# Performance work log

Measured on AMD Instinct MI355X. Metric: run time of the kernel, lower is better.

Reference implementation:

```python
import jax, jax.numpy as jnp
import numpy as np

K = 50  # hard-coded top-k in the original module


def setup_inputs() -> dict:
    key = jax.random.key(0)
    k1, k2 = jax.random.split(key)
    N = 16777216  # 2**24
    logit = jax.random.uniform(k1, (N,), dtype=jnp.float32)
    mv = jax.random.uniform(k2, (N,), dtype=jnp.float32)
    return {"logit": logit, "mv": mv}


def reference(logit, mv):
    dt = logit.dtype
    l1 = jnp.abs(logit - mv)
    _, idx = jax.lax.top_k(mv, K)

    # rank weights: base (detached mv + 0.5)*0.5; top-k entries scaled by
    # 2 * (((k - i)/k)**3 * 4 + 1) where i is the rank position.
    rank_w = (jax.lax.stop_gradient(mv) + 0.5) * 0.5
    ranks = jnp.arange(K, dtype=dt)
    factor = 2.0 * (((K - ranks) / K) ** 3 * 4.0 + 1.0)
    rank_w = rank_w.at[idx].multiply(factor)

    # gate: 1 if logit < mv else 1 if |logit-mv| > 0.1 else 0
    gate = jnp.where(logit < mv, jnp.ones((), dt), (l1 > 0.1).astype(dt))
    rank_loss = gate * rank_w * l1

    # pairwise gap loss over the k top indices (vectorized k x k)
    lt = logit[idx]                      # [K]
    diff = lt[:, None] - lt[None, :]     # [K, K], diff[i,j] = lt[i]-lt[j]
    upper = jnp.triu(jnp.ones((K, K), dtype=bool), 1)  # i < j
    pair_mask = upper & (jnp.abs(diff) < 0.05)
    gap = jnp.sum(jnp.where(pair_mask, jnp.maximum(jnp.zeros((), dt), 0.1 - diff), jnp.zeros((), dt)))
    num = jnp.sum(pair_mask)
    gap_loss = gap / jnp.maximum(1, num).astype(dt)

    return jnp.mean(rank_loss) + gap_loss
```

## Files before the change

### kernel.cpp

```cpp
#include <hip/hip_runtime.h>


#define NBLK  2048
#define NTHR  256
#define TILE  1024
#define ITERS 2
#define CAP   1024
#define KPT   (CAP / NTHR)
#define KTOP  50
#define TH    0.99997f

__device__ double             g_part[NBLK];
__device__ unsigned long long g_cand[CAP];

typedef const __attribute__((address_space(1))) void* gas_ptr;
typedef __attribute__((address_space(3))) void*       las_ptr;

__device__ __forceinline__ void dma16(const void* g, void* l) {
    __builtin_amdgcn_global_load_lds((gas_ptr)g, (las_ptr)l, 16, 0, 0);
}

__global__ __launch_bounds__(NTHR) void pass1(const float4* __restrict__ lg4,
                                              const float4* __restrict__ mv4,
                                              unsigned int* __restrict__ cnt) {
    __shared__ float4 s_lg[TILE];
    __shared__ float4 s_mv[TILE];
    const int tid  = threadIdx.x;
    const int lane = tid & 63;
    const int wv   = tid >> 6;

    float sum = 0.f;
    for (int it = 0; it < ITERS; ++it) {
        const int tb = (blockIdx.x * ITERS + it) * TILE;
        if (it) __syncthreads();
        #pragma unroll
        for (int k = 0; k < 4; ++k) {
            const int chunk = (wv * 4 + k) * 64;
            dma16(&lg4[tb + chunk + lane], &s_lg[chunk]);
        }
        #pragma unroll
        for (int k = 0; k < 4; ++k) {
            const int chunk = (wv * 4 + k) * 64;
            dma16(&mv4[tb + chunk + lane], &s_mv[chunk]);
        }
        __syncthreads();

        #pragma unroll
        for (int j = 0; j < TILE / NTHR; ++j) {
            const int pos = tid + j * NTHR;
            float4 l4 = s_lg[pos];
            float4 m4 = s_mv[pos];
            #pragma unroll
            for (int c = 0; c < 4; ++c) {
                float lv = (&l4.x)[c];
                float mv = (&m4.x)[c];
                float d  = fabsf(lv - mv);
                if ((lv < mv) || (d > 0.1f)) sum += (mv + 0.5f) * 0.5f * d;
                if (mv >= TH) {
                    unsigned p = atomicAdd(cnt, 1u);
                    if (p < CAP) {
                        unsigned idx = (unsigned)(4 * (tb + pos) + c);
                        g_cand[p] = ((unsigned long long)__float_as_uint(mv) << 32)
                                  | (unsigned long long)(~idx);
                    }
                }
            }
        }
    }

    __shared__ float s_red[NTHR / 64];
    #pragma unroll
    for (int o = 32; o > 0; o >>= 1) sum += __shfl_down(sum, o, 64);
    if ((tid & 63) == 0) s_red[wv] = sum;
    __syncthreads();
    if (tid == 0) {
        float t = 0.f;
        #pragma unroll
        for (int w = 0; w < NTHR / 64; ++w) t += s_red[w];
        g_part[blockIdx.x] = (double)t;
    }
}

__global__ __launch_bounds__(NTHR) void finalize(const float* __restrict__ lg,
                                                 float* __restrict__ out,
                                                 const unsigned int* __restrict__ cnt,
                                                 int n) {
    __shared__ double             s_dred[NTHR / 64];
    __shared__ unsigned long long s_keys[CAP];
    __shared__ float              s_mv[KTOP];
    __shared__ int                s_idx[KTOP];
    __shared__ float              s_lt[KTOP];
    __shared__ float              s_f[NTHR / 64];
    __shared__ int                s_i[NTHR / 64];
    __shared__ float              s_corr;
    const int tid = threadIdx.x;

    double ds = 0.0;
    #pragma unroll
    for (int t = 0; t < NBLK / NTHR; ++t) ds += g_part[tid + t * NTHR];
    #pragma unroll
    for (int o = 32; o > 0; o >>= 1) ds += __shfl_down(ds, o, 64);
    if ((tid & 63) == 0) s_dred[tid >> 6] = ds;

    unsigned C = *cnt;
    if (C > CAP) C = CAP;
    for (int i = tid; i < CAP; i += NTHR) s_keys[i] = (i < (int)C) ? g_cand[i] : 0ull;
    __syncthreads();

    unsigned long long own[KPT];
    int rank[KPT];
    #pragma unroll
    for (int t = 0; t < KPT; ++t) { own[t] = s_keys[tid + t * NTHR]; rank[t] = 0; }
    for (unsigned j = 0; j < C; ++j) {
        unsigned long long kj = s_keys[j];
        #pragma unroll
        for (int t = 0; t < KPT; ++t) rank[t] += (kj > own[t]) ? 1 : 0;
    }
    #pragma unroll
    for (int t = 0; t < KPT; ++t) {
        unsigned i = (unsigned)tid + (unsigned)t * NTHR;
        if (i < C && rank[t] < KTOP) {
            s_mv[rank[t]]  = __uint_as_float((unsigned)(own[t] >> 32));
            s_idx[rank[t]] = (int)(~(unsigned)own[t]);
        }
    }
    __syncthreads();

    if (tid < KTOP) s_lt[tid] = lg[s_idx[tid]];
    __syncthreads();

    float corr = 0.f;
    if (tid < KTOP) {
        float l = s_lt[tid], m = s_mv[tid];
        float d = fabsf(l - m);
        bool gate = (l < m) || (d > 0.1f);
        float r  = (float)(KTOP - tid) / (float)KTOP;
        float fk = 2.0f * (r * r * r * 4.0f + 1.0f);
        if (gate) corr = (m + 0.5f) * 0.5f * d * (fk - 1.0f);
    }
    #pragma unroll
    for (int o = 32; o > 0; o >>= 1) corr += __shfl_down(corr, o, 64);
    if (tid == 0) s_corr = corr;

    float gap = 0.f;
    int   num = 0;
    for (int p = tid; p < KTOP * KTOP; p += NTHR) {
        int i = p / KTOP, j = p % KTOP;
        if (i < j) {
            float diff = s_lt[i] - s_lt[j];
            if (fabsf(diff) < 0.05f) {
                float v = 0.1f - diff;
                gap += (v > 0.f) ? v : 0.f;
                num += 1;
            }
        }
    }
    #pragma unroll
    for (int o = 32; o > 0; o >>= 1) {
        gap += __shfl_down(gap, o, 64);
        num += __shfl_down(num, o, 64);
    }
    if ((tid & 63) == 0) { s_f[tid >> 6] = gap; s_i[tid >> 6] = num; }
    __syncthreads();

    if (tid == 0) {
        double bs = 0.0;
        float  gp = 0.f;
        int    nm = 0;
        #pragma unroll
        for (int w = 0; w < NTHR / 64; ++w) { bs += s_dred[w]; gp += s_f[w]; nm += s_i[w]; }
        float mean = (float)((bs + (double)s_corr) / (double)n);
        if (nm < 1) nm = 1;
        out[0] = mean + gp / (float)nm;
    }
}

extern "C" void kernel_launch(void* const* d_in, const int* in_sizes, int n_in,
                              void* d_out, int out_size, void* d_ws, size_t ws_size,
                              hipStream_t stream) {
    const float* logit = (const float*)d_in[0];
    const float* mv    = (const float*)d_in[1];
    float* out = (float*)d_out;
    unsigned int* cnt = (unsigned int*)d_ws;
    int n = in_sizes[0];

    hipMemsetAsync(cnt, 0, sizeof(unsigned int), stream);
    pass1<<<NBLK, NTHR, 0, stream>>>((const float4*)logit, (const float4*)mv, cnt);
    finalize<<<1, NTHR, 0, stream>>>(logit, out, cnt, n);
}
```

Measured before the change: 161.8 us.

## Double-buffer per-wave LDS DMA loads with waitcnt instead of block barriers

Each wave now owns a private, double-buffered slice of LDS and prefetches its next 128 float4 chunk of both inputs via global_load_lds while it computes on the current one. Block-wide __syncthreads inside the loop is replaced by a per-wave s_waitcnt on vmcnt. The goal is to overlap memory latency with compute and remove barrier stalls. It depends on the hand-coded waitcnt encoding being correct for LDS-DMA completion, and it shrinks the per-iteration tile, so there are more loop iterations.

```diff
diff --git a/kernel.cpp b/kernel.cpp
--- a/kernel.cpp
+++ b/kernel.cpp
@@ -3,12 +3,14 @@
 
 #define NBLK  2048
 #define NTHR  256
-#define TILE  1024
-#define ITERS 2
+#define ITERS 4
 #define CAP   1024
 #define KPT   (CAP / NTHR)
 #define KTOP  50
 #define TH    0.99997f
+
+#define WAIT_VM(n) do { __builtin_amdgcn_s_waitcnt(0x0F70 | (n)); \
+                        __builtin_amdgcn_sched_barrier(0); } while (0)
 
 __device__ double             g_part[NBLK];
 __device__ unsigned long long g_cand[CAP];
@@ -23,33 +25,39 @@
 __global__ __launch_bounds__(NTHR) void pass1(const float4* __restrict__ lg4,
                                               const float4* __restrict__ mv4,
                                               unsigned int* __restrict__ cnt) {
-    __shared__ float4 s_lg[TILE];
-    __shared__ float4 s_mv[TILE];
+    __shared__ float4 s_lg[2][4][128];
+    __shared__ float4 s_mv[2][4][128];
     const int tid  = threadIdx.x;
     const int lane = tid & 63;
     const int wv   = tid >> 6;
+    const int wbase = (blockIdx.x * 4 + wv) * (ITERS * 128);
+
+    #pragma unroll
+    for (int c = 0; c < 2; ++c) {
+        dma16(&lg4[wbase + c * 64 + lane], &s_lg[0][wv][c * 64]);
+        dma16(&mv4[wbase + c * 64 + lane], &s_mv[0][wv][c * 64]);
+    }
 
     float sum = 0.f;
+    int buf = 0;
     for (int it = 0; it < ITERS; ++it) {
-        const int tb = (blockIdx.x * ITERS + it) * TILE;
-        if (it) __syncthreads();
-        #pragma unroll
-        for (int k = 0; k < 4; ++k) {
-            const int chunk = (wv * 4 + k) * 64;
-            dma16(&lg4[tb + chunk + lane], &s_lg[chunk]);
+        if (it + 1 < ITERS) {
+            const int nb = wbase + (it + 1) * 128;
+            #pragma unroll
+            for (int c = 0; c < 2; ++c) {
+                dma16(&lg4[nb + c * 64 + lane], &s_lg[buf ^ 1][wv][c * 64]);
+                dma16(&mv4[nb + c * 64 + lane], &s_mv[buf ^ 1][wv][c * 64]);
+            }
+            WAIT_VM(4);
+        } else {
+            WAIT_VM(0);
         }
-        #pragma unroll
-        for (int k = 0; k < 4; ++k) {
-            const int chunk = (wv * 4 + k) * 64;
-            dma16(&mv4[tb + chunk + lane], &s_mv[chunk]);
-        }
-        __syncthreads();
 
         #pragma unroll
-        for (int j = 0; j < TILE / NTHR; ++j) {
-            const int pos = tid + j * NTHR;
-            float4 l4 = s_lg[pos];
-            float4 m4 = s_mv[pos];
+        for (int j = 0; j < 2; ++j) {
+            const int pos = j * 64 + lane;
+            float4 l4 = s_lg[buf][wv][pos];
+            float4 m4 = s_mv[buf][wv][pos];
             #pragma unroll
             for (int c = 0; c < 4; ++c) {
                 float lv = (&l4.x)[c];
@@ -59,19 +67,20 @@
                 if (mv >= TH) {
                     unsigned p = atomicAdd(cnt, 1u);
                     if (p < CAP) {
-                        unsigned idx = (unsigned)(4 * (tb + pos) + c);
+                        unsigned idx = (unsigned)(4 * (wbase + it * 128 + pos) + c);
                         g_cand[p] = ((unsigned long long)__float_as_uint(mv) << 32)
                                   | (unsigned long long)(~idx);
                     }
                 }
             }
         }
+        buf ^= 1;
     }
 
     __shared__ float s_red[NTHR / 64];
     #pragma unroll
     for (int o = 32; o > 0; o >>= 1) sum += __shfl_down(sum, o, 64);
-    if ((tid & 63) == 0) s_red[wv] = sum;
+    if (lane == 0) s_red[wv] = sum;
     __syncthreads();
     if (tid == 0) {
         float t = 0.f;
```

After: 162.8 us. Within noise of the previous version (+0.6%).
